# Kernel optimization log

Hardware: AMD Instinct MI355X
Metric: run time of the kernel (lower is better)

Reference implementation:

```python
import jax, jax.numpy as jnp
import numpy as np

N_NODES = 100000
N_EDGES = 3200000
IN_FEATS = 512
HIDDEN = 64
N_CLASSES = 32


def setup_inputs() -> dict:
    key = jax.random.key(0)
    k1, k2, k3, k4 = jax.random.split(key, 4)
    x = jax.random.normal(k1, (N_NODES, IN_FEATS), dtype=jnp.float32)
    edge_index = jax.random.randint(k2, (2, N_EDGES), 0, N_NODES, dtype=jnp.int64)
    # Glorot-ish init for weights
    W1 = jax.random.normal(k3, (IN_FEATS, HIDDEN), dtype=jnp.float32) / np.sqrt(IN_FEATS)
    b1 = jnp.zeros((HIDDEN,), dtype=jnp.float32)
    W2 = jax.random.normal(k4, (HIDDEN, N_CLASSES), dtype=jnp.float32) / np.sqrt(HIDDEN)
    b2 = jnp.zeros((N_CLASSES,), dtype=jnp.float32)
    return {"x": x, "edge_index": edge_index, "W1": W1, "b1": b1, "W2": W2, "b2": b2}


def reference(x, edge_index, W1, b1, W2, b2):
    N = x.shape[0]
    # GCNConv default: add self-loops, unit edge weights (edge_attr is None for Cora)
    loop = jnp.arange(N, dtype=edge_index.dtype)
    src = jnp.concatenate([edge_index[0], loop])  # [E+N]
    dst = jnp.concatenate([edge_index[1], loop])  # [E+N]
    w = jnp.ones(src.shape[0], dtype=x.dtype)
    # symmetric normalization: deg^-1/2[src] * w * deg^-1/2[dst]
    deg = jax.ops.segment_sum(w, dst, num_segments=N)
    dinv = jnp.where(deg > 0, jax.lax.rsqrt(deg), 0.0)
    norm = dinv[src] * w * dinv[dst]  # [E+N]

    def gcn_layer(h, W, b):
        h = h @ W                              # transform first (out dim small)
        msg = h[src] * norm[:, None]           # gather + scale  [E+N, d_out]
        agg = jax.ops.segment_sum(msg, dst, num_segments=N)  # scatter-add
        return agg + b

    h = jax.nn.relu(gcn_layer(x, W1, b1))
    # F.dropout(training=self.training) -> identity in eval mode
    out = gcn_layer(h, W2, b2)
    return jax.nn.log_softmax(out, axis=1)
```

## Files before the change

### kernel.cpp

```cpp
#include <hip/hip_runtime.h>
#include <hip/hip_fp16.h>
#include <math.h>

constexpr int N_NODES = 100000;
constexpr int N_EDGES = 3200000;
constexpr int IN_F = 512;
constexpr int HID = 64;
constexpr int NCLS = 32;
constexpr int CAP = 80;
constexpr int SHIFT = 9;
constexpr int NB = 196;
constexpr int BCAPC = 16976;
constexpr int CHUNK = 2048;
constexpr int SENT = N_NODES;

constexpr int GEMM1_BLOCKS = (N_NODES + 63) / 64;
constexpr int PART_BLOCKS  = (N_EDGES + CHUNK - 1) / CHUNK;

typedef short short8 __attribute__((ext_vector_type(8)));
typedef float f32x4 __attribute__((ext_vector_type(4)));
typedef int intx4 __attribute__((ext_vector_type(4)));

__device__ __forceinline__ unsigned short f2bf(float f) {
    union { float f; unsigned int u; } v; v.f = f;
    unsigned int r = (v.u + 0x7fffu + ((v.u >> 16) & 1u)) >> 16;
    return (unsigned short)r;
}
__device__ __forceinline__ float bf2f(unsigned short h) {
    union { unsigned int u; float f; } v; v.u = ((unsigned int)h) << 16;
    return v.f;
}
__device__ __forceinline__ unsigned char f2e5(float f) {
    unsigned short u = __half_as_ushort(__float2half(f));
    return (unsigned char)((u + 0x7Fu + ((u >> 8) & 1u)) >> 8);
}
__device__ __forceinline__ float e52f(unsigned char b) {
    return __half2float(__ushort_as_half((unsigned short)((unsigned short)b << 8)));
}

__global__ __launch_bounds__(256) void k_prep(const float* __restrict__ W1,
                                              unsigned short* __restrict__ W1T,
                                              unsigned char* __restrict__ h1s,
                                              unsigned char* __restrict__ h2s,
                                              int* __restrict__ gtail) {
    if (blockIdx.x == 128) {
        int t = threadIdx.x;
        if (t < HID)  h1s[(size_t)SENT * HID + t] = 0;
        if (t < NCLS) h2s[(size_t)SENT * NCLS + t] = 0;
        for (int i = t; i < NB * 16; i += 256) gtail[i] = 0;
        return;
    }
    int t = blockIdx.x * 256 + threadIdx.x;
    int k = t >> 6, c = t & 63;
    W1T[(size_t)c * IN_F + k] = f2bf(W1[(size_t)k * HID + c]);
}


__global__ __launch_bounds__(256) void k_part_gemm1(const int* __restrict__ src,
                                                    const int* __restrict__ dst,
                                                    int* __restrict__ gtail,
                                                    int* __restrict__ recs,
                                                    const float* __restrict__ x,
                                                    const unsigned short* __restrict__ W1T,
                                                    unsigned short* __restrict__ h1) {
    __shared__ alignas(16) char smem[20608];
    const int tid = threadIdx.x;
    const int wid = blockIdx.x >> 1;
    const int lane = tid & 63;
    if (blockIdx.x & 1) {
        int* buf            = (int*)smem;
        unsigned char* bbuf = (unsigned char*)(smem + 8192);
        int* loc   = (int*)(smem + 10240);
        int* lh    = (int*)(smem + 11328);
        int* lbase = (int*)(smem + 12352);
        int* wsum  = (int*)(smem + 13376);
        const int wv = tid >> 6;
        const int c0 = wid * CHUNK;
        const int cnum = min(CHUNK, N_EDGES - c0);
        lh[tid] = 0;
        __syncthreads();
        int dd[8], ss[8], rk[8];
        #pragma unroll
        for (int k = 0; k < 8; ++k) {
            int i = k * 256 + tid;
            if (i < cnum) {
                dd[k] = dst[c0 + i];
                ss[k] = src[c0 + i];
                rk[k] = atomicAdd(&lh[dd[k] >> SHIFT], 1);
            }
        }
        __syncthreads();
        int orig = lh[tid];
        int v = orig;
        #pragma unroll
        for (int off = 1; off < 64; off <<= 1) {
            int t = __shfl_up(v, off, 64);
            if (lane >= off) v += t;
        }
        if (lane == 63) wsum[wv] = v;
        __syncthreads();
        int pre = 0;
        #pragma unroll
        for (int k = 0; k < 4; ++k) if (k < wv) pre += wsum[k];
        int incl = v + pre;
        loc[tid] = incl - orig;
        if (tid == 255) loc[256] = incl;
        if (tid < NB && orig > 0) lbase[tid] = atomicAdd(&gtail[tid * 16], orig);
        __syncthreads();
        #pragma unroll
        for (int k = 0; k < 8; ++k) {
            int i = k * 256 + tid;
            if (i < cnum) {
                int b = dd[k] >> SHIFT;
                int pos = loc[b] + rk[k];
                buf[pos] = ((dd[k] & 511) << 17) | ss[k];
                bbuf[pos] = (unsigned char)b;
            }
        }
        __syncthreads();
        for (int i = tid; i < cnum; i += 256) {
            int b = bbuf[i];
            int idx = lbase[b] + (i - loc[b]);
            if (idx < BCAPC) recs[(size_t)b * BCAPC + idx] = buf[i];
        }
        return;
    }
    short* Xb = (short*)smem;
    short* Wb = (short*)(smem + 10240);
    const int row0 = wid * 64;
    const int w = tid >> 6;
    const int r0l = (w >> 1) * 32;
    const int c0l = (w & 1) * 32;
    const int lrow = lane & 15;
    const int lkb = (lane >> 4) << 3;
    const int sr = tid >> 2;
    const int skq = (tid & 3) << 3;
    f32x4 acc00 = {0.f, 0.f, 0.f, 0.f}, acc01 = acc00, acc10 = acc00, acc11 = acc00;

    const int grow = row0 + sr;
    const bool valid = grow < N_NODES;
    const float* xp0 = &x[(size_t)grow * IN_F + skq];
    const unsigned short* wp0 = &W1T[(size_t)sr * IN_F + skq];

    float4 v0 = make_float4(0.f, 0.f, 0.f, 0.f), v1 = v0;
    if (valid) { v0 = *reinterpret_cast<const float4*>(xp0);
                 v1 = *reinterpret_cast<const float4*>(xp0 + 4); }
    short8 wa = *reinterpret_cast<const short8*>(wp0);

    #pragma unroll 4
    for (int s = 0; s < 16; ++s) {
        const int p = (s & 1) * 2560;
        short8 px;
        px[0] = (short)f2bf(v0.x); px[1] = (short)f2bf(v0.y);
        px[2] = (short)f2bf(v0.z); px[3] = (short)f2bf(v0.w);
        px[4] = (short)f2bf(v1.x); px[5] = (short)f2bf(v1.y);
        px[6] = (short)f2bf(v1.z); px[7] = (short)f2bf(v1.w);
        *reinterpret_cast<short8*>(&Xb[p + sr * 40 + skq]) = px;
        *reinterpret_cast<short8*>(&Wb[p + sr * 40 + skq]) = wa;
        __syncthreads();
        if (s < 15) {
            const float* xp = xp0 + (s + 1) * 32;
            if (valid) { v0 = *reinterpret_cast<const float4*>(xp);
                         v1 = *reinterpret_cast<const float4*>(xp + 4); }
            wa = *reinterpret_cast<const short8*>(wp0 + (s + 1) * 32);
        }
        short8 a0 = *reinterpret_cast<const short8*>(&Xb[p + (r0l + lrow) * 40 + lkb]);
        short8 a1 = *reinterpret_cast<const short8*>(&Xb[p + (r0l + 16 + lrow) * 40 + lkb]);
        short8 b0 = *reinterpret_cast<const short8*>(&Wb[p + (c0l + lrow) * 40 + lkb]);
        short8 b1 = *reinterpret_cast<const short8*>(&Wb[p + (c0l + 16 + lrow) * 40 + lkb]);
        acc00 = __builtin_amdgcn_mfma_f32_16x16x32_bf16(a0, b0, acc00, 0, 0, 0);
        acc01 = __builtin_amdgcn_mfma_f32_16x16x32_bf16(a0, b1, acc01, 0, 0, 0);
        acc10 = __builtin_amdgcn_mfma_f32_16x16x32_bf16(a1, b0, acc10, 0, 0, 0);
        acc11 = __builtin_amdgcn_mfma_f32_16x16x32_bf16(a1, b1, acc11, 0, 0, 0);
    }
    const int vr0 = row0 + r0l + ((lane >> 4) << 2);
    const int gc0 = c0l + (lane & 15);
    #pragma unroll
    for (int v = 0; v < 4; ++v) {
        int gr = vr0 + v;
        if (gr < N_NODES) {
            h1[(size_t)gr * HID + gc0]      = f2bf(acc00[v]);
            h1[(size_t)gr * HID + gc0 + 16] = f2bf(acc01[v]);
        }
        int gr2 = gr + 16;
        if (gr2 < N_NODES) {
            h1[(size_t)gr2 * HID + gc0]      = f2bf(acc10[v]);
            h1[(size_t)gr2 * HID + gc0 + 16] = f2bf(acc11[v]);
        }
    }
}


__global__ __launch_bounds__(1024) void k_phase2(const int* __restrict__ gtail,
                                                 const int* __restrict__ recs,
                                                 int* __restrict__ slots,
                                                 int* __restrict__ cnt,
                                                 float* __restrict__ dinv,
                                                 const unsigned short* __restrict__ h1,
                                                 unsigned char* __restrict__ h1s) {
    __shared__ int scnt[512];
    const int b = blockIdx.x;
    const int tid = threadIdx.x;
    if (tid < 512) scnt[tid] = 0;
    __syncthreads();
    int nrec = min(gtail[b * 16], BCAPC);
    const int* rb = recs + (size_t)b * BCAPC;
    for (int i = tid; i < nrec; i += 1024) {
        int r = rb[i];
        int ln = r >> 17;
        int s  = r & 0x1FFFF;
        int p = atomicAdd(&scnt[ln], 1);
        int node = (b << SHIFT) + ln;
        if (p < CAP) slots[(size_t)node * CAP + p] = s;
    }
    __syncthreads();
    if (tid < 512) {
        int node = (b << SHIFT) + tid;
        if (node < N_NODES) {
            int c = scnt[tid];
            cnt[node] = c;
            dinv[node] = rsqrtf(1.0f + (float)c);
            int c2 = min(c, CAP);
            int degp = (c2 + 15) & ~15;
            for (int p = c2; p < degp; ++p) slots[(size_t)node * CAP + p] = SENT;
        }
    }
    for (int idx = tid; idx < 512 * 8; idx += 1024) {
        int ln = idx >> 3, g = idx & 7;
        int node = (b << SHIFT) + ln;
        if (node >= N_NODES) continue;
        float dv = rsqrtf(1.0f + (float)scnt[ln]);
        const unsigned short* hr = h1 + (size_t)node * HID;
        unsigned char* hs = h1s + (size_t)node * HID;
        short8 hv = *reinterpret_cast<const short8*>(hr + g * 8);
        unsigned int lo = 0, hi = 0;
        #pragma unroll
        for (int e = 0; e < 4; ++e)
            lo |= (unsigned int)f2e5(bf2f((unsigned short)hv[e]) * dv) << (e * 8);
        #pragma unroll
        for (int e = 0; e < 4; ++e)
            hi |= (unsigned int)f2e5(bf2f((unsigned short)hv[4 + e]) * dv) << (e * 8);
        *reinterpret_cast<uint2*>(hs + g * 8) = make_uint2(lo, hi);
    }
}


__global__ __launch_bounds__(256) void k_gather1(const int* __restrict__ cnt,
                                                 const int* __restrict__ slots,
                                                 const float* __restrict__ dinv,
                                                 const unsigned char* __restrict__ h1s,
                                                 const float* __restrict__ b1,
                                                 const float* __restrict__ W2,
                                                 unsigned char* __restrict__ h2s) {
    __shared__ alignas(16) float hsh[4][64];
    const int lane = threadIdx.x & 63;
    const int wv = threadIdx.x >> 6;
    const int cls = lane & 31;
    const int half = lane >> 5;
    float w[32];
    #pragma unroll
    for (int j = 0; j < 32; ++j)
        w[j] = W2[(size_t)(half * 32 + j) * NCLS + cls];
    const float bb = b1[lane];
    const int nw = gridDim.x * 4;
    for (int n0 = blockIdx.x * 4 + wv; n0 < N_NODES; n0 += nw) {
        const int n = __builtin_amdgcn_readfirstlane(n0);
        float dn = dinv[n];
        int deg = min(cnt[n], CAP);
        int degp = (deg + 15) & ~15;
        size_t base = (size_t)n * CAP;
        float a0 = e52f(h1s[(((unsigned)n) << 6) + lane]);
        float a1 = 0.f, a2 = 0.f, a3 = 0.f, a4 = 0.f, a5 = 0.f, a6 = 0.f, a7 = 0.f;
        for (int j = 0; j < degp; j += 16) {
            intx4 sa = __builtin_nontemporal_load(reinterpret_cast<const intx4*>(&slots[base + j]));
            intx4 sb = __builtin_nontemporal_load(reinterpret_cast<const intx4*>(&slots[base + j + 4]));
            intx4 sc = __builtin_nontemporal_load(reinterpret_cast<const intx4*>(&slots[base + j + 8]));
            intx4 sd = __builtin_nontemporal_load(reinterpret_cast<const intx4*>(&slots[base + j + 12]));
            a0 += e52f(h1s[(((unsigned)sa.x) << 6) + lane]);
            a1 += e52f(h1s[(((unsigned)sa.y) << 6) + lane]);
            a2 += e52f(h1s[(((unsigned)sa.z) << 6) + lane]);
            a3 += e52f(h1s[(((unsigned)sa.w) << 6) + lane]);
            a4 += e52f(h1s[(((unsigned)sb.x) << 6) + lane]);
            a5 += e52f(h1s[(((unsigned)sb.y) << 6) + lane]);
            a6 += e52f(h1s[(((unsigned)sb.z) << 6) + lane]);
            a7 += e52f(h1s[(((unsigned)sb.w) << 6) + lane]);
            a0 += e52f(h1s[(((unsigned)sc.x) << 6) + lane]);
            a1 += e52f(h1s[(((unsigned)sc.y) << 6) + lane]);
            a2 += e52f(h1s[(((unsigned)sc.z) << 6) + lane]);
            a3 += e52f(h1s[(((unsigned)sc.w) << 6) + lane]);
            a4 += e52f(h1s[(((unsigned)sd.x) << 6) + lane]);
            a5 += e52f(h1s[(((unsigned)sd.y) << 6) + lane]);
            a6 += e52f(h1s[(((unsigned)sd.z) << 6) + lane]);
            a7 += e52f(h1s[(((unsigned)sd.w) << 6) + lane]);
        }
        float v = fmaf(((a0 + a1) + (a2 + a3)) + ((a4 + a5) + (a6 + a7)), dn, bb);
        v = fmaxf(v, 0.f);
        hsh[wv][lane] = v;
        float acc = 0.f;
        #pragma unroll
        for (int q = 0; q < 8; ++q) {
            f32x4 hv = *reinterpret_cast<const f32x4*>(&hsh[wv][half * 32 + q * 4]);
            acc = fmaf(hv.x, w[q * 4 + 0], acc);
            acc = fmaf(hv.y, w[q * 4 + 1], acc);
            acc = fmaf(hv.z, w[q * 4 + 2], acc);
            acc = fmaf(hv.w, w[q * 4 + 3], acc);
        }
        acc += __shfl_xor(acc, 32, 64);
        if (half == 0)
            h2s[(((unsigned)n) << 5) + cls] = f2e5(acc * dn);
    }
}


__global__ __launch_bounds__(256) void k_out(const int* __restrict__ cnt,
                                             const int* __restrict__ slots,
                                             const float* __restrict__ dinv,
                                             const unsigned char* __restrict__ h2s,
                                             const float* __restrict__ b2,
                                             float* __restrict__ out) {
    int wid = blockIdx.x * 4 + (threadIdx.x >> 6);
    int n = __builtin_amdgcn_readfirstlane(wid);
    if (n >= N_NODES) return;
    int lane = threadIdx.x & 63;
    int cls = lane & 31;
    int half = lane >> 5;
    float dn = dinv[n];
    int deg = min(cnt[n], CAP);
    int degp = (deg + 15) & ~15;
    size_t base = (size_t)n * CAP;
    float a0 = half ? 0.f : e52f(h2s[(((unsigned)n) << 5) + cls]);
    float a1 = 0.f, a2 = 0.f, a3 = 0.f;
    for (int j = 0; j < degp; j += 16) {
        intx4 s0 = __builtin_nontemporal_load(
            reinterpret_cast<const intx4*>(&slots[base + j + half * 8]));
        intx4 s1 = __builtin_nontemporal_load(
            reinterpret_cast<const intx4*>(&slots[base + j + half * 8 + 4]));
        a0 += e52f(h2s[(((unsigned)s0.x) << 5) + cls]);
        a1 += e52f(h2s[(((unsigned)s0.y) << 5) + cls]);
        a2 += e52f(h2s[(((unsigned)s0.z) << 5) + cls]);
        a3 += e52f(h2s[(((unsigned)s0.w) << 5) + cls]);
        a0 += e52f(h2s[(((unsigned)s1.x) << 5) + cls]);
        a1 += e52f(h2s[(((unsigned)s1.y) << 5) + cls]);
        a2 += e52f(h2s[(((unsigned)s1.z) << 5) + cls]);
        a3 += e52f(h2s[(((unsigned)s1.w) << 5) + cls]);
    }
    float acc = (a0 + a1) + (a2 + a3);
    acc += __shfl_xor(acc, 32, 64);
    float z = fmaf(acc, dn, b2[cls]);
    float mx = z;
    #pragma unroll
    for (int d = 16; d > 0; d >>= 1) mx = fmaxf(mx, __shfl_xor(mx, d, 32));
    float ex = expf(z - mx);
    float sm = ex;
    #pragma unroll
    for (int d = 16; d > 0; d >>= 1) sm += __shfl_xor(sm, d, 32);
    if (half == 0)
        out[(size_t)n * NCLS + cls] = z - mx - logf(sm);
}


extern "C" void kernel_launch(void* const* d_in, const int* in_sizes, int n_in,
                              void* d_out, int out_size, void* d_ws, size_t ws_size,
                              hipStream_t stream) {
    const float* x  = (const float*)d_in[0];
    const int*   ei = (const int*)d_in[1];
    const float* W1 = (const float*)d_in[2];
    const float* b1 = (const float*)d_in[3];
    const float* W2 = (const float*)d_in[4];
    const float* b2 = (const float*)d_in[5];
    float* out = (float*)d_out;
    char* ws = (char*)d_ws;

    const int* src = ei;
    const int* dst = ei + N_EDGES;

    int*   gtail = (int*)ws;
    int*   cnt   = (int*)(ws + 16384);
    float* dinv  = (float*)(ws + 416384);
    unsigned short* W1T = (unsigned short*)(ws + 816384);
    int*   slots = (int*)(ws + 881920);
    unsigned short* h1 = (unsigned short*)(ws + 32882048ull);
    unsigned char* h1s = (unsigned char*)(ws + 45682048ull);
    char*  recs_base   = ws + 52082176ull;
    int*   recs  = (int*)recs_base;
    unsigned char* h2s  = (unsigned char*)(ws + 65391360ull);

    k_prep<<<129, 256, 0, stream>>>(W1, W1T, h1s, h2s, gtail);
    k_part_gemm1<<<GEMM1_BLOCKS + PART_BLOCKS, 256, 0, stream>>>(src, dst, gtail, recs, x, W1T, h1);
    k_phase2<<<NB, 1024, 0, stream>>>(gtail, recs, slots, cnt, dinv, h1, h1s);
    k_gather1<<<1536, 256, 0, stream>>>(cnt, slots, dinv, h1s, b1, W2, h2s);
    k_out<<<(N_NODES + 3) / 4, 256, 0, stream>>>(cnt, slots, dinv, h2s, b2, out);
}
```

Baseline: 205.2 us.

## Load X operands directly into registers for GEMM1, skipping LDS staging

The GEMM1 path now has each lane load its own MFMA A-operand rows of x straight from global memory into registers and convert them to bf16 there, so x no longer goes through shared memory. Only W1T is still staged in LDS. Global loads are double-buffered two k-steps ahead, the loop is fully unrolled, and LDS drops from 20608 to 13904 bytes, which may allow more blocks per CU. In exchange each row is read with scattered 32-byte segments per lane instead of coalesced tile loads, register pressure goes up, and every wave that shares a row reloads the same x data.

```diff
diff --git a/kernel.cpp b/kernel.cpp
--- a/kernel.cpp
+++ b/kernel.cpp
@@ -63,7 +63,7 @@
                                                     const float* __restrict__ x,
                                                     const unsigned short* __restrict__ W1T,
                                                     unsigned short* __restrict__ h1) {
-    __shared__ alignas(16) char smem[20608];
+    __shared__ alignas(16) char smem[13904];
     const int tid = threadIdx.x;
     const int wid = blockIdx.x >> 1;
     const int lane = tid & 63;
@@ -125,47 +125,59 @@
         }
         return;
     }
-    short* Xb = (short*)smem;
-    short* Wb = (short*)(smem + 10240);
+    short* Wb = (short*)smem;
     const int row0 = wid * 64;
     const int w = tid >> 6;
     const int r0l = (w >> 1) * 32;
     const int c0l = (w & 1) * 32;
     const int lrow = lane & 15;
     const int lkb = (lane >> 4) << 3;
-    const int sr = tid >> 2;
-    const int skq = (tid & 3) << 3;
     f32x4 acc00 = {0.f, 0.f, 0.f, 0.f}, acc01 = acc00, acc10 = acc00, acc11 = acc00;
 
-    const int grow = row0 + sr;
-    const bool valid = grow < N_NODES;
-    const float* xp0 = &x[(size_t)grow * IN_F + skq];
-    const unsigned short* wp0 = &W1T[(size_t)sr * IN_F + skq];
-
-    float4 v0 = make_float4(0.f, 0.f, 0.f, 0.f), v1 = v0;
-    if (valid) { v0 = *reinterpret_cast<const float4*>(xp0);
-                 v1 = *reinterpret_cast<const float4*>(xp0 + 4); }
-    short8 wa = *reinterpret_cast<const short8*>(wp0);
-
-    #pragma unroll 4
+    int rA = min(row0 + r0l + lrow, N_NODES - 1);
+    int rB = min(row0 + r0l + 16 + lrow, N_NODES - 1);
+    const float* xA = x + (size_t)rA * IN_F + lkb;
+    const float* xB = x + (size_t)rB * IN_F + lkb;
+
+    const int wrow = tid >> 2;
+    const int wchk = (tid & 3) << 3;
+    const unsigned short* wp = W1T + (size_t)wrow * IN_F + wchk;
+
+    short8 wa = *reinterpret_cast<const short8*>(wp);
+    float4 A0lo[2], A0hi[2], A1lo[2], A1hi[2];
+    A0lo[0] = *reinterpret_cast<const float4*>(xA);
+    A0hi[0] = *reinterpret_cast<const float4*>(xA + 4);
+    A1lo[0] = *reinterpret_cast<const float4*>(xB);
+    A1hi[0] = *reinterpret_cast<const float4*>(xB + 4);
+    A0lo[1] = *reinterpret_cast<const float4*>(xA + 32);
+    A0hi[1] = *reinterpret_cast<const float4*>(xA + 36);
+    A1lo[1] = *reinterpret_cast<const float4*>(xB + 32);
+    A1hi[1] = *reinterpret_cast<const float4*>(xB + 36);
+
+    #pragma unroll
     for (int s = 0; s < 16; ++s) {
         const int p = (s & 1) * 2560;
-        short8 px;
-        px[0] = (short)f2bf(v0.x); px[1] = (short)f2bf(v0.y);
-        px[2] = (short)f2bf(v0.z); px[3] = (short)f2bf(v0.w);
-        px[4] = (short)f2bf(v1.x); px[5] = (short)f2bf(v1.y);
-        px[6] = (short)f2bf(v1.z); px[7] = (short)f2bf(v1.w);
-        *reinterpret_cast<short8*>(&Xb[p + sr * 40 + skq]) = px;
-        *reinterpret_cast<short8*>(&Wb[p + sr * 40 + skq]) = wa;
-        __syncthreads();
-        if (s < 15) {
-            const float* xp = xp0 + (s + 1) * 32;
-            if (valid) { v0 = *reinterpret_cast<const float4*>(xp);
-                         v1 = *reinterpret_cast<const float4*>(xp + 4); }
-            wa = *reinterpret_cast<const short8*>(wp0 + (s + 1) * 32);
-        }
-        short8 a0 = *reinterpret_cast<const short8*>(&Xb[p + (r0l + lrow) * 40 + lkb]);
-        short8 a1 = *reinterpret_cast<const short8*>(&Xb[p + (r0l + 16 + lrow) * 40 + lkb]);
+        *reinterpret_cast<short8*>(&Wb[p + wrow * 40 + wchk]) = wa;
+        asm volatile("s_waitcnt lgkmcnt(0)" ::: "memory");
+        __builtin_amdgcn_s_barrier();
+        if (s < 15) wa = *reinterpret_cast<const short8*>(wp + (s + 1) * 32);
+        float4 c0lo = A0lo[s & 1], c0hi = A0hi[s & 1];
+        float4 c1lo = A1lo[s & 1], c1hi = A1hi[s & 1];
+        if (s < 14) {
+            A0lo[s & 1] = *reinterpret_cast<const float4*>(xA + (s + 2) * 32);
+            A0hi[s & 1] = *reinterpret_cast<const float4*>(xA + (s + 2) * 32 + 4);
+            A1lo[s & 1] = *reinterpret_cast<const float4*>(xB + (s + 2) * 32);
+            A1hi[s & 1] = *reinterpret_cast<const float4*>(xB + (s + 2) * 32 + 4);
+        }
+        short8 a0, a1;
+        a0[0] = (short)f2bf(c0lo.x); a0[1] = (short)f2bf(c0lo.y);
+        a0[2] = (short)f2bf(c0lo.z); a0[3] = (short)f2bf(c0lo.w);
+        a0[4] = (short)f2bf(c0hi.x); a0[5] = (short)f2bf(c0hi.y);
+        a0[6] = (short)f2bf(c0hi.z); a0[7] = (short)f2bf(c0hi.w);
+        a1[0] = (short)f2bf(c1lo.x); a1[1] = (short)f2bf(c1lo.y);
+        a1[2] = (short)f2bf(c1lo.z); a1[3] = (short)f2bf(c1lo.w);
+        a1[4] = (short)f2bf(c1hi.x); a1[5] = (short)f2bf(c1hi.y);
+        a1[6] = (short)f2bf(c1hi.z); a1[7] = (short)f2bf(c1hi.w);
         short8 b0 = *reinterpret_cast<const short8*>(&Wb[p + (c0l + lrow) * 40 + lkb]);
         short8 b1 = *reinterpret_cast<const short8*>(&Wb[p + (c0l + 16 + lrow) * 40 + lkb]);
         acc00 = __builtin_amdgcn_mfma_f32_16x16x32_bf16(a0, b0, acc00, 0, 0, 0);
```

Result: slower. 250.3 us (+22.0%).
